# Optimization experiments

Hardware: AMD Instinct MI355X
Metric: run time of the kernel (lower is better)

The kernel has to match this reference:

```python
import jax, jax.numpy as jnp
import numpy as np

GROUP_SIZE = 7
ROI_SCALE = 1.3
BIN_SCALE = 1.5


def setup_inputs() -> dict:
    key = jax.random.key(0)
    k1, k2, k3, k4 = jax.random.split(key, 4)
    B, C, H, W = 2, 490, 128, 128  # C = output_dim(10) * group_size(7)**2
    N = 512
    stride = 16
    features = jax.random.normal(k1, (B, C, H, W), dtype=jnp.float32)
    img_w = W * stride
    bidx = jax.random.randint(k2, (N, 1), 0, B).astype(jnp.float32)
    xy1 = jax.random.uniform(k3, (N, 2), minval=0.0, maxval=img_w - 64.0)
    wh = jax.random.uniform(k4, (N, 2), minval=32.0, maxval=512.0)
    xy2 = jnp.minimum(xy1 + wh, img_w - 1.0)
    rois = jnp.concatenate([bidx, xy1[:, 0:1], xy1[:, 1:2], xy2[:, 0:1], xy2[:, 1:2]], axis=1)
    return {"rois": rois, "features": features, "stride": stride}


def reference(rois, features, stride):
    G = GROUP_SIZE
    B, C, H, W = features.shape
    D = C // (G * G)  # output_dim, computed dynamically as in the torch module
    dt = features.dtype
    spatial_scale = 1.0 / stride

    rois = rois[:, :5].astype(dt)
    batch_idx = rois[:, 0].astype(jnp.int32)  # [N]
    # rounded roi corners in feature-map coordinates (end is inclusive +1)
    rsw = jnp.round(rois[:, 1]) * spatial_scale
    rsh = jnp.round(rois[:, 2]) * spatial_scale
    rew = (jnp.round(rois[:, 3]) + 1.0) * spatial_scale
    reh = (jnp.round(rois[:, 4]) + 1.0) * spatial_scale
    # mask (context) enlargement around roi center by ROI_SCALE
    rw, rh = rew - rsw, reh - rsh
    rwm, rhm = rw * ROI_SCALE, rh * ROI_SCALE
    swm = (rsw + rew) * 0.5 - rwm * 0.5
    shm = (rsh + reh) * 0.5 - rhm * 0.5
    rwm = jnp.maximum(rwm, 0.1)  # force tiny rois to 1x1
    rhm = jnp.maximum(rhm, 0.1)
    bin_h = rhm / G  # [N]
    bin_w = rwm / G
    dh = bin_h * (BIN_SCALE - 1.0) * 0.5  # extra bin context
    dw = bin_w * (BIN_SCALE - 1.0) * 0.5

    g = jnp.arange(G, dtype=dt)  # bin index
    hstart = jnp.clip(jnp.floor(shm[:, None] + g[None, :] * bin_h[:, None] - dh[:, None]), 0, H).astype(jnp.int32)  # [N,G]
    hend = jnp.clip(jnp.ceil(shm[:, None] + (g[None, :] + 1.0) * bin_h[:, None] + dh[:, None]), 0, H).astype(jnp.int32)
    wstart = jnp.clip(jnp.floor(swm[:, None] + g[None, :] * bin_w[:, None] - dw[:, None]), 0, W).astype(jnp.int32)
    wend = jnp.clip(jnp.ceil(swm[:, None] + (g[None, :] + 1.0) * bin_w[:, None] + dw[:, None]), 0, W).astype(jnp.int32)

    # integral image so each bin-average is 4 gathers instead of a dynamic loop
    cs = jnp.cumsum(jnp.cumsum(features, axis=2), axis=3)
    S = jnp.pad(cs, ((0, 0), (0, 0), (1, 0), (1, 0)))  # [B,C,H+1,W+1]
    # position-sensitive channel map c = (d*G + ph)*G + pw  <=>  reshape C -> [D,G,G]
    Sr = S.reshape(B, D, G, G, H + 1, W + 1)

    N = rois.shape[0]
    b_ = batch_idx[:, None, None, None]          # [N,1,1,1]
    d_ = jnp.arange(D)[None, :, None, None]      # [1,D,1,1]
    pi = jnp.arange(G)[None, None, :, None]      # [1,1,G,1] (ph)
    pj = jnp.arange(G)[None, None, None, :]      # [1,1,1,G] (pw)
    hs = hstart[:, None, :, None]
    he = hend[:, None, :, None]
    ws = wstart[:, None, None, :]
    we = wend[:, None, None, :]

    total = (Sr[b_, d_, pi, pj, he, we] - Sr[b_, d_, pi, pj, hs, we]
             - Sr[b_, d_, pi, pj, he, ws] + Sr[b_, d_, pi, pj, hs, ws])  # [N,D,G,G]

    area = ((hend - hstart)[:, None, :, None] * (wend - wstart)[:, None, None, :])  # [N,1->D,G,G] via broadcast
    area = jnp.broadcast_to(area, total.shape)
    out = jnp.where(area > 0, total / jnp.maximum(area, 1).astype(dt), jnp.zeros((), dt))
    return out
```

## Files before the change

### kernel.cpp

```cpp
#include <hip/hip_runtime.h>

#define GS   7
#define CCH  490
#define HH   128
#define WW   128
#define LDW  132
#define NB   2

typedef float v2f __attribute__((ext_vector_type(2)));

__global__ __launch_bounds__(512, 4) void psroi_fused(
    const float* __restrict__ rois,
    const float* __restrict__ feat,
    const int*   __restrict__ stride_p,
    float*       __restrict__ out)
{
#pragma clang fp contract(off)
    __shared__ float S[HH * LDW];

    const int bc = blockIdx.x;
    const int b  = bc / CCH;
    const int c  = bc - b * CCH;
    const float* __restrict__ f = feat + (size_t)bc * (HH * WW);
    const int tid = threadIdx.x;

    {
        const int c2 = tid & 63;
        const int sg = tid >> 6;
        const int r0 = sg * 16;

        v2f v[16];
        const v2f* fp = (const v2f*)(f + r0 * WW) + c2;
        #pragma unroll
        for (int i = 0; i < 16; ++i)
            v[i] = fp[i * (WW / 2)];
        #pragma unroll
        for (int i = 1; i < 16; ++i)
            v[i] += v[i - 1];

        *(v2f*)&S[sg * LDW + 2 * c2] = v[15];
        __syncthreads();
        v2f off = {0.0f, 0.0f};
        #pragma unroll
        for (int s = 0; s < 7; ++s)
            if (sg > s) off += *(const v2f*)&S[s * LDW + 2 * c2];
        __syncthreads();

        float* sp = &S[r0 * LDW + 2 * c2];
        #pragma unroll
        for (int i = 0; i < 16; ++i) {
            v2f q = v[i] + off;
            *(v2f*)&sp[i * LDW] = q;
        }
    }
    __syncthreads();

    {
        const int row = tid >> 2;
        const int ws_ = tid & 3;
        float* rp = &S[row * LDW + ws_ * 32];

        float u[32];
        #pragma unroll
        for (int i = 0; i < 8; ++i) {
            const float4 q = *(const float4*)&rp[i * 4];
            u[4 * i + 0] = q.x; u[4 * i + 1] = q.y;
            u[4 * i + 2] = q.z; u[4 * i + 3] = q.w;
        }
        #pragma unroll
        for (int i = 1; i < 32; ++i)
            u[i] += u[i - 1];

        const float tot = u[31];
        const float t1 = __shfl_up(tot, 1, 64);
        const float t2 = __shfl_up(tot, 2, 64);
        const float t3 = __shfl_up(tot, 3, 64);
        float off = 0.0f;
        if (ws_ > 0) off += t1;
        if (ws_ > 1) off += t2;
        if (ws_ > 2) off += t3;

        #pragma unroll
        for (int i = 0; i < 8; ++i) {
            float4 q;
            q.x = u[4 * i + 0] + off; q.y = u[4 * i + 1] + off;
            q.z = u[4 * i + 2] + off; q.w = u[4 * i + 3] + off;
            *(float4*)&rp[i * 4] = q;
        }
    }
    __syncthreads();

    {
        const int n = tid;
        const float b_f = rois[n * 5 + 0];
        const int bi = (int)b_f;
        if (bi == b) {
            const float ss = 1.0f / (float)(*stride_p);
            const int d   = c / (GS * GS);
            const int rem = c - d * (GS * GS);
            const int pi  = rem / GS;
            const int pj  = rem - pi * GS;

            const float x1 = rois[n * 5 + 1];
            const float y1 = rois[n * 5 + 2];
            const float x2 = rois[n * 5 + 3];
            const float y2 = rois[n * 5 + 4];

            float rsw = rintf(x1) * ss;
            float rsh = rintf(y1) * ss;
            float rew = (rintf(x2) + 1.0f) * ss;
            float reh = (rintf(y2) + 1.0f) * ss;
            float rwv = rew - rsw;
            float rhv = reh - rsh;
            float rwm = rwv * 1.3f;
            float rhm = rhv * 1.3f;
            float swm = (rsw + rew) * 0.5f - rwm * 0.5f;
            float shm = (rsh + reh) * 0.5f - rhm * 0.5f;
            rwm = fmaxf(rwm, 0.1f);
            rhm = fmaxf(rhm, 0.1f);
            float bin_h = rhm / 7.0f;
            float bin_w = rwm / 7.0f;
            float dh = bin_h * 0.25f;
            float dw = bin_w * 0.25f;

            const float gi = (float)pi;
            const float gj = (float)pj;
            const int hs  = (int)fminf(fmaxf(floorf(shm + gi * bin_h - dh),          0.0f), 128.0f);
            const int he  = (int)fminf(fmaxf(ceilf (shm + (gi + 1.0f) * bin_h + dh), 0.0f), 128.0f);
            const int ws2 = (int)fminf(fmaxf(floorf(swm + gj * bin_w - dw),          0.0f), 128.0f);
            const int we  = (int)fminf(fmaxf(ceilf (swm + (gj + 1.0f) * bin_w + dw), 0.0f), 128.0f);

            const int area = (he - hs) * (we - ws2);
            const float A  = (he > 0 && we  > 0) ? S[(he - 1) * LDW + (we  - 1)] : 0.0f;
            const float Bv = (hs > 0 && we  > 0) ? S[(hs - 1) * LDW + (we  - 1)] : 0.0f;
            const float Cv = (he > 0 && ws2 > 0) ? S[(he - 1) * LDW + (ws2 - 1)] : 0.0f;
            const float Dv = (hs > 0 && ws2 > 0) ? S[(hs - 1) * LDW + (ws2 - 1)] : 0.0f;
            const float total = ((A - Bv) - Cv) + Dv;
            out[(size_t)n * CCH + c] = (area > 0) ? (total / (float)area) : 0.0f;
        }
    }
}

extern "C" void kernel_launch(void* const* d_in, const int* in_sizes, int n_in,
                              void* d_out, int out_size, void* d_ws, size_t ws_size,
                              hipStream_t stream)
{
    const float* rois     = (const float*)d_in[0];
    const float* feat     = (const float*)d_in[1];
    const int*   stride_p = (const int*)d_in[2];
    float*       out      = (float*)d_out;

    dim3 grid(NB * CCH);
    dim3 block(512);
    hipLaunchKernelGGL(psroi_fused, grid, block, 0, stream, rois, feat, stride_p, out);
}
```

Before: 98.97 us.

## Split integral image into two row halves to halve LDS and raise occupancy

The integral image is built in two 64-row halves that reuse a half-sized LDS buffer. The carry row from the first half seeds the second half's column prefix, and the pooling reads for each half are gathered in between. This halves shared memory per block so launch bounds can request 8 waves per SIMD. The second half's global loads are issued before the first half is consumed, the ROI geometry is computed up front, and __syncthreads is replaced by a raw waitcnt plus s_barrier. The cost is more barriers and an extra prefix pass, plus some dead shuffle code left in the row-scan phase.

New measurement: 99.91 us. About the same (+0.9%).

```diff
diff --git a/kernel.cpp b/kernel.cpp
--- a/kernel.cpp
+++ b/kernel.cpp
@@ -4,19 +4,25 @@
 #define CCH  490
 #define HH   128
 #define WW   128
-#define LDW  132
+#define HALF 64
+#define LDW  140
 #define NB   2
 
 typedef float v2f __attribute__((ext_vector_type(2)));
 
-__global__ __launch_bounds__(512, 4) void psroi_fused(
+__device__ __forceinline__ void bar_lds() {
+    asm volatile("s_waitcnt lgkmcnt(0)" ::: "memory");
+    __builtin_amdgcn_s_barrier();
+}
+
+__global__ __launch_bounds__(512, 8) void psroi_fused(
     const float* __restrict__ rois,
     const float* __restrict__ feat,
     const int*   __restrict__ stride_p,
     float*       __restrict__ out)
 {
 #pragma clang fp contract(off)
-    __shared__ float S[HH * LDW];
+    __shared__ float S[HALF * LDW];
 
     const int bc = blockIdx.x;
     const int b  = bc / CCH;
@@ -24,120 +30,179 @@
     const float* __restrict__ f = feat + (size_t)bc * (HH * WW);
     const int tid = threadIdx.x;
 
-    {
-        const int c2 = tid & 63;
-        const int sg = tid >> 6;
-        const int r0 = sg * 16;
-
-        v2f v[16];
-        const v2f* fp = (const v2f*)(f + r0 * WW) + c2;
-        #pragma unroll
-        for (int i = 0; i < 16; ++i)
-            v[i] = fp[i * (WW / 2)];
-        #pragma unroll
-        for (int i = 1; i < 16; ++i)
-            v[i] += v[i - 1];
-
-        *(v2f*)&S[sg * LDW + 2 * c2] = v[15];
-        __syncthreads();
-        v2f off = {0.0f, 0.0f};
-        #pragma unroll
-        for (int s = 0; s < 7; ++s)
-            if (sg > s) off += *(const v2f*)&S[s * LDW + 2 * c2];
-        __syncthreads();
-
-        float* sp = &S[r0 * LDW + 2 * c2];
-        #pragma unroll
-        for (int i = 0; i < 16; ++i) {
-            v2f q = v[i] + off;
-            *(v2f*)&sp[i * LDW] = q;
-        }
-    }
-    __syncthreads();
-
-    {
-        const int row = tid >> 2;
-        const int ws_ = tid & 3;
-        float* rp = &S[row * LDW + ws_ * 32];
-
-        float u[32];
-        #pragma unroll
-        for (int i = 0; i < 8; ++i) {
+    const int c2 = tid & 63;
+    const int sg = tid >> 6;
+    float* sp = &S[(sg * 8) * LDW + 2 * c2];
+
+    v2f va[8];
+    {
+        const v2f* fp = (const v2f*)(f + (sg * 8) * WW) + c2;
+        #pragma unroll
+        for (int i = 0; i < 8; ++i)
+            va[i] = fp[i * (WW / 2)];
+    }
+
+    const int n = tid;
+    const int bi = (int)rois[n * 5 + 0];
+    const float ss = 1.0f / (float)(*stride_p);
+    {
+    }
+    const int d   = c / (GS * GS);
+    const int rem = c - d * (GS * GS);
+    const int pi  = rem / GS;
+    const int pj  = rem - pi * GS;
+
+    const float x1 = rois[n * 5 + 1];
+    const float y1 = rois[n * 5 + 2];
+    const float x2 = rois[n * 5 + 3];
+    const float y2 = rois[n * 5 + 4];
+
+    float rsw = rintf(x1) * ss;
+    float rsh = rintf(y1) * ss;
+    float rew = (rintf(x2) + 1.0f) * ss;
+    float reh = (rintf(y2) + 1.0f) * ss;
+    float rwv = rew - rsw;
+    float rhv = reh - rsh;
+    float rwm = rwv * 1.3f;
+    float rhm = rhv * 1.3f;
+    float swm = (rsw + rew) * 0.5f - rwm * 0.5f;
+    float shm = (rsh + reh) * 0.5f - rhm * 0.5f;
+    rwm = fmaxf(rwm, 0.1f);
+    rhm = fmaxf(rhm, 0.1f);
+    float bin_h = rhm / 7.0f;
+    float bin_w = rwm / 7.0f;
+    float dh = bin_h * 0.25f;
+    float dw = bin_w * 0.25f;
+
+    const float gi = (float)pi;
+    const float gj = (float)pj;
+    const int hs  = (int)fminf(fmaxf(floorf(shm + gi * bin_h - dh),          0.0f), 128.0f);
+    const int he  = (int)fminf(fmaxf(ceilf (shm + (gi + 1.0f) * bin_h + dh), 0.0f), 128.0f);
+    const int ws2 = (int)fminf(fmaxf(floorf(swm + gj * bin_w - dw),          0.0f), 128.0f);
+    const int we  = (int)fminf(fmaxf(ceilf (swm + (gj + 1.0f) * bin_w + dw), 0.0f), 128.0f);
+    const int area = (he - hs) * (we - ws2);
+    const bool act = (bi == b);
+
+    auto phaseB = [&]() {
+#pragma clang fp contract(off)
+        const int row = tid >> 3;
+        const int s8  = tid & 7;
+        float* rp = &S[row * LDW + s8 * 16];
+
+        float u[16];
+        #pragma unroll
+        for (int i = 0; i < 4; ++i) {
             const float4 q = *(const float4*)&rp[i * 4];
             u[4 * i + 0] = q.x; u[4 * i + 1] = q.y;
             u[4 * i + 2] = q.z; u[4 * i + 3] = q.w;
         }
         #pragma unroll
-        for (int i = 1; i < 32; ++i)
+        for (int i = 1; i < 16; ++i)
             u[i] += u[i - 1];
 
-        const float tot = u[31];
+        const float tot = u[15];
+        float off = 0.0f;
+        #pragma unroll
+        for (int k = 1; k < 8; ++k) {
+            const float tk = __shfl_up(tot, k, 64);
+            if (s8 > k - 1 && k <= s8) off += 0.0f;
+        }
+        off = 0.0f;
         const float t1 = __shfl_up(tot, 1, 64);
         const float t2 = __shfl_up(tot, 2, 64);
         const float t3 = __shfl_up(tot, 3, 64);
-        float off = 0.0f;
-        if (ws_ > 0) off += t1;
-        if (ws_ > 1) off += t2;
-        if (ws_ > 2) off += t3;
-
-        #pragma unroll
-        for (int i = 0; i < 8; ++i) {
+        const float t4 = __shfl_up(tot, 4, 64);
+        const float t5 = __shfl_up(tot, 5, 64);
+        const float t6 = __shfl_up(tot, 6, 64);
+        const float t7 = __shfl_up(tot, 7, 64);
+        if (s8 > 6) off += t7;
+        if (s8 > 5) off += t6;
+        if (s8 > 4) off += t5;
+        if (s8 > 3) off += t4;
+        if (s8 > 2) off += t3;
+        if (s8 > 1) off += t2;
+        if (s8 > 0) off += t1;
+
+        bar_lds();
+        #pragma unroll
+        for (int i = 0; i < 4; ++i) {
             float4 q;
             q.x = u[4 * i + 0] + off; q.y = u[4 * i + 1] + off;
             q.z = u[4 * i + 2] + off; q.w = u[4 * i + 3] + off;
             *(float4*)&rp[i * 4] = q;
         }
-    }
-    __syncthreads();
-
-    {
-        const int n = tid;
-        const float b_f = rois[n * 5 + 0];
-        const int bi = (int)b_f;
-        if (bi == b) {
-            const float ss = 1.0f / (float)(*stride_p);
-            const int d   = c / (GS * GS);
-            const int rem = c - d * (GS * GS);
-            const int pi  = rem / GS;
-            const int pj  = rem - pi * GS;
-
-            const float x1 = rois[n * 5 + 1];
-            const float y1 = rois[n * 5 + 2];
-            const float x2 = rois[n * 5 + 3];
-            const float y2 = rois[n * 5 + 4];
-
-            float rsw = rintf(x1) * ss;
-            float rsh = rintf(y1) * ss;
-            float rew = (rintf(x2) + 1.0f) * ss;
-            float reh = (rintf(y2) + 1.0f) * ss;
-            float rwv = rew - rsw;
-            float rhv = reh - rsh;
-            float rwm = rwv * 1.3f;
-            float rhm = rhv * 1.3f;
-            float swm = (rsw + rew) * 0.5f - rwm * 0.5f;
-            float shm = (rsh + reh) * 0.5f - rhm * 0.5f;
-            rwm = fmaxf(rwm, 0.1f);
-            rhm = fmaxf(rhm, 0.1f);
-            float bin_h = rhm / 7.0f;
-            float bin_w = rwm / 7.0f;
-            float dh = bin_h * 0.25f;
-            float dw = bin_w * 0.25f;
-
-            const float gi = (float)pi;
-            const float gj = (float)pj;
-            const int hs  = (int)fminf(fmaxf(floorf(shm + gi * bin_h - dh),          0.0f), 128.0f);
-            const int he  = (int)fminf(fmaxf(ceilf (shm + (gi + 1.0f) * bin_h + dh), 0.0f), 128.0f);
-            const int ws2 = (int)fminf(fmaxf(floorf(swm + gj * bin_w - dw),          0.0f), 128.0f);
-            const int we  = (int)fminf(fmaxf(ceilf (swm + (gj + 1.0f) * bin_w + dw), 0.0f), 128.0f);
-
-            const int area = (he - hs) * (we - ws2);
-            const float A  = (he > 0 && we  > 0) ? S[(he - 1) * LDW + (we  - 1)] : 0.0f;
-            const float Bv = (hs > 0 && we  > 0) ? S[(hs - 1) * LDW + (we  - 1)] : 0.0f;
-            const float Cv = (he > 0 && ws2 > 0) ? S[(he - 1) * LDW + (ws2 - 1)] : 0.0f;
-            const float Dv = (hs > 0 && ws2 > 0) ? S[(hs - 1) * LDW + (ws2 - 1)] : 0.0f;
-            const float total = ((A - Bv) - Cv) + Dv;
-            out[(size_t)n * CCH + c] = (area > 0) ? (total / (float)area) : 0.0f;
-        }
+    };
+
+    float Av = 0.0f, Bv = 0.0f, Cv = 0.0f, Dv = 0.0f;
+    auto pool_reads = [&](int lo) {
+        if (act) {
+            if (he > 0 && we  > 0 && (he - 1) >= lo && (he - 1) < lo + HALF)
+                Av = S[(he - 1 - lo) * LDW + (we - 1)];
+            if (hs > 0 && we  > 0 && (hs - 1) >= lo && (hs - 1) < lo + HALF)
+                Bv = S[(hs - 1 - lo) * LDW + (we - 1)];
+            if (he > 0 && ws2 > 0 && (he - 1) >= lo && (he - 1) < lo + HALF)
+                Cv = S[(he - 1 - lo) * LDW + (ws2 - 1)];
+            if (hs > 0 && ws2 > 0 && (hs - 1) >= lo && (hs - 1) < lo + HALF)
+                Dv = S[(hs - 1 - lo) * LDW + (ws2 - 1)];
+        }
+    };
+
+    #pragma unroll
+    for (int i = 1; i < 8; ++i) va[i] += va[i - 1];
+    *(v2f*)&S[sg * LDW + 2 * c2] = va[7];
+    bar_lds();
+    {
+        v2f off = {0.0f, 0.0f};
+        #pragma unroll
+        for (int s = 0; s < 7; ++s)
+            if (sg > s) off += *(const v2f*)&S[s * LDW + 2 * c2];
+        bar_lds();
+        #pragma unroll
+        for (int i = 0; i < 8; ++i) {
+            v2f q = va[i] + off;
+            *(v2f*)&sp[i * LDW] = q;
+        }
+    }
+
+    v2f vb[8];
+    {
+        const v2f* fp = (const v2f*)(f + (HALF + sg * 8) * WW) + c2;
+        #pragma unroll
+        for (int i = 0; i < 8; ++i)
+            vb[i] = fp[i * (WW / 2)];
+    }
+
+    bar_lds();
+    const v2f cr = *(const v2f*)&S[63 * LDW + 2 * c2];
+    phaseB();
+    bar_lds();
+    pool_reads(0);
+    bar_lds();
+
+    #pragma unroll
+    for (int i = 1; i < 8; ++i) vb[i] += vb[i - 1];
+    *(v2f*)&S[sg * LDW + 2 * c2] = vb[7];
+    bar_lds();
+    {
+        v2f off = cr;
+        #pragma unroll
+        for (int s = 0; s < 7; ++s)
+            if (sg > s) off += *(const v2f*)&S[s * LDW + 2 * c2];
+        bar_lds();
+        #pragma unroll
+        for (int i = 0; i < 8; ++i) {
+            v2f q = vb[i] + off;
+            *(v2f*)&sp[i * LDW] = q;
+        }
+    }
+    bar_lds();
+    phaseB();
+    bar_lds();
+    pool_reads(HALF);
+
+    if (act) {
+        const float total = ((Av - Bv) - Cv) + Dv;
+        out[(size_t)n * CCH + c] = (area > 0) ? (total / (float)area) : 0.0f;
     }
 }
 
```
